# Optimization experiments

Measured on AMD Instinct MI355X. Metric: run time of the kernel, lower is better.

## Reference

```python
import jax, jax.numpy as jnp
import numpy as np

B, F, C, H, W = 4, 16, 768, 16, 16   # video: b f c h w
L, M = 64, 16                        # audio: b c l m
NH = 12                              # num_heads
WS_V = 4                             # local_window (video window size, frames)
GROUPS = 32                          # GroupNorm32
EPS = 1e-5


def group_norm(x, scale, bias):
    # x: [b, c, t]; normalize over (channels-within-group, t)
    b, c, t = x.shape
    xg = x.reshape(b, GROUPS, c // GROUPS, t)
    mu = xg.mean(axis=(2, 3), keepdims=True)
    var = xg.var(axis=(2, 3), keepdims=True)
    xg = (xg - mu) * jax.lax.rsqrt(var + EPS)
    return xg.reshape(b, c, t) * scale[None, :, None] + bias[None, :, None]


def setup_inputs() -> dict:
    key = jax.random.key(0)
    ks = jax.random.split(key, 8)
    s = 0.02
    return {
        "video": jax.random.normal(ks[0], (B, F, C, H, W), jnp.float32),
        "audio": jax.random.normal(ks[1], (B, C, L, M), jnp.float32),
        "vn_scale": jnp.ones((C,), jnp.float32),
        "vn_bias": jnp.zeros((C,), jnp.float32),
        "an_scale": jnp.ones((C,), jnp.float32),
        "an_bias": jnp.zeros((C,), jnp.float32),
        "vqkv_w": jax.random.normal(ks[2], (3 * C, C), jnp.float32) * s,
        "vqkv_b": jnp.zeros((3 * C,), jnp.float32),
        "aqkv_w": jax.random.normal(ks[3], (3 * C, C), jnp.float32) * s,
        "aqkv_b": jnp.zeros((3 * C,), jnp.float32),
        "vproj_w": jax.random.normal(ks[4], (C, C), jnp.float32) * s,  # zero_module in orig; random for nontrivial baseline
        "vproj_b": jnp.zeros((C,), jnp.float32),
        "aproj_w": jax.random.normal(ks[5], (C, C), jnp.float32) * s,
        "aproj_b": jnp.zeros((C,), jnp.float32),
    }


def reference(video, audio, vn_scale, vn_bias, an_scale, an_bias,
              vqkv_w, vqkv_b, aqkv_w, aqkv_b,
              vproj_w, vproj_b, aproj_w, aproj_b):
    b, f, c, h, w = video.shape
    _, _, l, m = audio.shape
    ch = c // NH
    scale = ch ** -0.25
    ws_audio = WS_V * l // f
    nwin = f // WS_V
    wsv_tok = WS_V * h * w      # video tokens per window
    wsa_tok = ws_audio * m      # audio tokens per window

    vt = jnp.transpose(video, (0, 2, 1, 3, 4)).reshape(b, c, f * h * w)  # b c (f h w)
    at = audio.reshape(b, c, l * m)                                       # b c (l m)

    # 1x1 conv qkv after GroupNorm
    vqkv = jnp.einsum('oc,bct->bot', vqkv_w, group_norm(vt, vn_scale, vn_bias)) + vqkv_b[None, :, None]
    aqkv = jnp.einsum('oc,bct->bot', aqkv_w, group_norm(at, an_scale, an_bias)) + aqkv_b[None, :, None]
    q_v, k_v, v_v = jnp.split(vqkv, 3, axis=1)
    q_a, k_a, v_a = jnp.split(aqkv, 3, axis=1)

    # attention_index with window_shift = 0
    va_index = (jnp.arange(wsa_tok)[None, :] + (jnp.arange(nwin) * wsa_tok)[:, None]) % (l * m)
    av_index = (jnp.arange(wsv_tok)[None, :] + (jnp.arange(nwin) * wsv_tok)[:, None]) % (f * h * w)

    def heads(x):
        return x.reshape(b, NH, ch, -1)

    # video queries attend gathered audio windows
    qv = heads(q_v).reshape(b, NH, ch, nwin, wsv_tok)
    ka = jnp.take(heads(k_a), va_index, axis=-1)   # [b,NH,ch,nwin,wsa_tok]
    vav = jnp.take(heads(v_a), va_index, axis=-1)
    wts = jax.nn.softmax(jnp.einsum('bhcnt,bhcns->bhnts', qv * scale, ka * scale), axis=-1)
    v_out = jnp.einsum('bhnts,bhcns->bhcnt', wts, vav).reshape(b, c, f * h * w)

    # audio queries attend gathered video windows
    qa = heads(q_a).reshape(b, NH, ch, nwin, wsa_tok)
    kv = jnp.take(heads(k_v), av_index, axis=-1)   # [b,NH,ch,nwin,wsv_tok]
    vvv = jnp.take(heads(v_v), av_index, axis=-1)
    wts = jax.nn.softmax(jnp.einsum('bhcnt,bhcns->bhnts', qa * scale, kv * scale), axis=-1)
    a_out = jnp.einsum('bhnts,bhcns->bhcnt', wts, vvv).reshape(b, c, l * m)

    # zero-init 1x1x1 / 1x1 proj_out convs + residual
    vh = jnp.transpose(v_out.reshape(b, c, f, h, w), (0, 2, 1, 3, 4))  # b f c h w
    vh = jnp.einsum('oc,bfchw->bfohw', vproj_w, vh) + vproj_b[None, None, :, None, None]
    ah = jnp.einsum('oc,bclm->bolm', aproj_w, a_out.reshape(b, c, l, m)) + aproj_b[None, :, None, None]
    return video + vh, audio + ah
```

## Files before the change

### kernel.cpp

```cpp
#include <hip/hip_runtime.h>
#include <hip/hip_bf16.h>

typedef unsigned short ushort_t;
typedef __attribute__((ext_vector_type(8))) short short8;
typedef __attribute__((ext_vector_type(4))) float f32x4;
struct __align__(8) us4 { ushort_t x, y, z, w; };

#define DI __device__ __forceinline__

DI float b2f(unsigned int u16) {
  union { unsigned int i; float f; } v;
  v.i = u16 << 16;
  return v.f;
}
DI ushort_t f2b(float f) {
  union { float f; unsigned int u; } v; v.f = f;
  unsigned int r = v.u + 0x7FFFu + ((v.u >> 16) & 1u);
  return (ushort_t)(r >> 16);
}

DI void gl_lds16(const ushort_t* g, ushort_t* l) {
  __builtin_amdgcn_global_load_lds(
      (const __attribute__((address_space(1))) unsigned int*)g,
      (__attribute__((address_space(3))) unsigned int*)l, 16, 0, 0);
}

__global__ __launch_bounds__(256) void fused_pre_kernel(
    const float* __restrict__ video, const float* __restrict__ audio,
    float* __restrict__ part,
    const float* __restrict__ w0, const float* __restrict__ w1,
    const float* __restrict__ w2, const float* __restrict__ w3,
    ushort_t* __restrict__ o0, ushort_t* __restrict__ o1,
    ushort_t* __restrict__ o2, ushort_t* __restrict__ o3) {
  const int bid = blockIdx.x;
  const int tid = threadIdx.x;
  __shared__ float red[8];
  if (bid < 2560) {
    float s = 0.f, ss = 0.f;
    if (bid < 2048) {
      int bg = bid >> 4, f = bid & 15;
      int b = bg >> 5, g = bg & 31;
      const float4* base = reinterpret_cast<const float4*>(
          video + ((size_t)((b * 16 + f) * 768 + g * 24)) * 256);
#pragma unroll
      for (int i = 0; i < 6; ++i) {
        float4 v = base[i * 256 + tid];
        s += v.x + v.y + v.z + v.w;
        ss += v.x * v.x + v.y * v.y + v.z * v.z + v.w * v.w;
      }
    } else {
      int a = bid - 2048;
      int bg = a >> 2, p = a & 3;
      int b = bg >> 5, g = bg & 31;
      const float* ab = audio + ((size_t)(b * 768 + g * 24)) * 1024 + p * 256;
#pragma unroll
      for (int i = 0; i < 6; ++i) {
        int row = i * 4 + (tid >> 6);
        float4 v = *reinterpret_cast<const float4*>(ab + (size_t)row * 1024 + (tid & 63) * 4);
        s += v.x + v.y + v.z + v.w;
        ss += v.x * v.x + v.y * v.y + v.z * v.z + v.w * v.w;
      }
    }
    for (int off = 32; off > 0; off >>= 1) { s += __shfl_down(s, off, 64); ss += __shfl_down(ss, off, 64); }
    int wv = tid >> 6, ln = tid & 63;
    if (ln == 0) { red[wv * 2] = s; red[wv * 2 + 1] = ss; }
    __syncthreads();
    if (tid == 0) {
      part[bid * 2] = red[0] + red[2] + red[4] + red[6];
      part[bid * 2 + 1] = red[1] + red[3] + red[5] + red[7];
    }
  } else {
    const int n1 = (2304 * 768) / 4, n3 = (768 * 768) / 4;
    const int total = 2 * n1 + 2 * n3;
    int wb = bid - 2560;
    for (int i = wb * 256 + tid; i < total; i += 1024 * 256) {
      const float4* src;
      ushort_t* dst;
      int j;
      if (i < n1) { src = (const float4*)w0; dst = o0; j = i; }
      else if (i < 2 * n1) { src = (const float4*)w1; dst = o1; j = i - n1; }
      else if (i < 2 * n1 + n3) { src = (const float4*)w2; dst = o2; j = i - 2 * n1; }
      else { src = (const float4*)w3; dst = o3; j = i - 2 * n1 - n3; }
      float4 v = src[j];
      us4 o = {f2b(v.x), f2b(v.y), f2b(v.z), f2b(v.w)};
      *reinterpret_cast<us4*>(dst + (size_t)j * 4) = o;
    }
  }
}

__global__ __launch_bounds__(256) void norm_fused_kernel(
    const float* __restrict__ video, const float* __restrict__ audio,
    const float* __restrict__ part,
    const float* __restrict__ vsc, const float* __restrict__ vbi,
    const float* __restrict__ asc, const float* __restrict__ abi,
    ushort_t* __restrict__ Xv, ushort_t* __restrict__ Xa) {
  __shared__ float T[32][257];
  __shared__ float shA[32], shB[32];
  const int bx = blockIdx.x;
  const int tid = threadIdx.x;
  if (bx < 1536) {
    const int bf = bx / 24, ct = bx % 24;
    const int b = bf >> 4, f = bf & 15;
    const int c0 = ct * 32;
    if (tid < 32) {
      int c = c0 + tid, g = c / 24;
      float s = 0.f, ss = 0.f;
#pragma unroll
      for (int i = 0; i < 16; ++i) {
        s += part[((b * 32 + g) * 16 + i) * 2];
        ss += part[((b * 32 + g) * 16 + i) * 2 + 1];
      }
      const float N = 24.f * 4096.f;
      float m = s / N;
      float r = rsqrtf(ss / N - m * m + 1e-5f);
      float A = r * vsc[c];
      shA[tid] = A;
      shB[tid] = vbi[c] - m * A;
    }
    __syncthreads();
#pragma unroll
    for (int i = 0; i < 8; ++i) {
      int idx = i * 256 + tid;
      int c = idx >> 6, q4 = idx & 63;
      float4 v = *reinterpret_cast<const float4*>(
          video + ((size_t)((b * 16 + f) * 768 + c0 + c)) * 256 + q4 * 4);
      float A = shA[c], B = shB[c];
      float4 o = {A * v.x + B, A * v.y + B, A * v.z + B, A * v.w + B};
      *reinterpret_cast<float4*>(&T[c][q4 * 4]) = o;
    }
    __syncthreads();
#pragma unroll
    for (int i = 0; i < 8; ++i) {
      int idx = i * 256 + tid;
      int c4 = idx & 7, hw = idx >> 3;
      us4 o = {f2b(T[c4 * 4 + 0][hw]), f2b(T[c4 * 4 + 1][hw]),
               f2b(T[c4 * 4 + 2][hw]), f2b(T[c4 * 4 + 3][hw])};
      *reinterpret_cast<us4*>(Xv + ((size_t)(b * 4096 + f * 256 + hw)) * 768 + c0 + c4 * 4) = o;
    }
  } else {
    const int ax = bx - 1536;
    const int bt = ax / 24, ct = ax % 24;
    const int b = bt >> 2, t0 = (bt & 3) * 256;
    const int c0 = ct * 32;
    if (tid < 32) {
      int c = c0 + tid, g = c / 24;
      float s = 0.f, ss = 0.f;
#pragma unroll
      for (int i = 0; i < 4; ++i) {
        s += part[(2048 + (b * 32 + g) * 4 + i) * 2];
        ss += part[(2048 + (b * 32 + g) * 4 + i) * 2 + 1];
      }
      const float N = 24.f * 1024.f;
      float m = s / N;
      float r = rsqrtf(ss / N - m * m + 1e-5f);
      float A = r * asc[c];
      shA[tid] = A;
      shB[tid] = abi[c] - m * A;
    }
    __syncthreads();
#pragma unroll
    for (int i = 0; i < 8; ++i) {
      int idx = i * 256 + tid;
      int c = idx >> 6, q4 = idx & 63;
      float4 v = *reinterpret_cast<const float4*>(
          audio + ((size_t)(b * 768 + c0 + c)) * 1024 + t0 + q4 * 4);
      float A = shA[c], B = shB[c];
      float4 o = {A * v.x + B, A * v.y + B, A * v.z + B, A * v.w + B};
      *reinterpret_cast<float4*>(&T[c][q4 * 4]) = o;
    }
    __syncthreads();
#pragma unroll
    for (int i = 0; i < 8; ++i) {
      int idx = i * 256 + tid;
      int c4 = idx & 7, tt = idx >> 3;
      us4 o = {f2b(T[c4 * 4 + 0][tt]), f2b(T[c4 * 4 + 1][tt]),
               f2b(T[c4 * 4 + 2][tt]), f2b(T[c4 * 4 + 3][tt])};
      *reinterpret_cast<us4*>(Xa + ((size_t)(b * 1024 + t0 + tt)) * 768 + c0 + c4 * 4) = o;
    }
  }
}

__global__ __launch_bounds__(256) void qkv_fused_kernel(
    const ushort_t* __restrict__ Xv, const ushort_t* __restrict__ Xa,
    const ushort_t* __restrict__ Wqv, const ushort_t* __restrict__ Wqa,
    const float* __restrict__ vqkv_b, const float* __restrict__ aqkv_b,
    ushort_t* __restrict__ Qv, ushort_t* __restrict__ Kv, ushort_t* __restrict__ Vv,
    ushort_t* __restrict__ Qa, ushort_t* __restrict__ Ka, ushort_t* __restrict__ Va) {
  __shared__ ushort_t sm[32768];
  const int bid = blockIdx.x;
  const int tid = threadIdx.x;
  const int lane = tid & 63, wave = tid >> 6;
  const int quad = lane >> 4, l16 = lane & 15;

  const bool isv = bid < 2304;
  const int lb = isv ? bid : bid - 2304;
  const int nwg = isv ? 2304 : 576;
  const ushort_t* A = isv ? Xv : Xa;
  const ushort_t* W = isv ? Wqv : Wqa;
  const float* bias = isv ? vqkv_b : aqkv_b;
  ushort_t* pQ = isv ? Qv : Qa;
  ushort_t* pK = isv ? Kv : Ka;
  ushort_t* pV = isv ? Vv : Va;
  const int M = isv ? 16384 : 4096;

  const int lid = (lb & 7) * (nwg >> 3) + (lb >> 3);
  const int n0 = (lid % 18) * 128, m0 = (lid / 18) * 128;
  const int wm = (wave & 1) * 64, wn = (wave >> 1) * 64;

  const int srow = wave * 32 + (lane >> 3);
  const int sq = ((lane & 7) ^ (lane >> 3)) * 8;
  const ushort_t* gA = A + (size_t)(m0 + srow) * 768 + sq;
  const ushort_t* gB = W + (size_t)(n0 + srow) * 768 + sq;

  f32x4 acc[4][4];
#pragma unroll
  for (int i = 0; i < 4; ++i)
#pragma unroll
    for (int j = 0; j < 4; ++j) acc[i][j] = (f32x4){0.f, 0.f, 0.f, 0.f};

  auto stage = [&](int kc, int cur) {
    ushort_t* lA = sm + cur * 8192 + wave * 2048;
    ushort_t* lB = sm + 16384 + cur * 8192 + wave * 2048;
#pragma unroll
    for (int i = 0; i < 4; ++i) {
      gl_lds16(gA + (size_t)i * 8 * 768 + kc, lA + i * 512);
      gl_lds16(gB + (size_t)i * 8 * 768 + kc, lB + i * 512);
    }
  };

  stage(0, 0);
  __syncthreads();
  int cur = 0;
  for (int t = 0; t < 12; ++t) {
    if (t < 11) stage((t + 1) * 64, cur ^ 1);
    const ushort_t* cA = sm + cur * 8192;
    const ushort_t* cB = sm + 16384 + cur * 8192;
#pragma unroll
    for (int ks = 0; ks < 2; ++ks) {
      short8 av[4], bv[4];
#pragma unroll
      for (int im = 0; im < 4; ++im) {
        int rr = wm + im * 16 + l16;
        av[im] = *reinterpret_cast<const short8*>(
            cA + rr * 64 + (((ks * 4 + quad) ^ (rr & 7)) * 8));
      }
#pragma unroll
      for (int in = 0; in < 4; ++in) {
        int rr = wn + in * 16 + l16;
        bv[in] = *reinterpret_cast<const short8*>(
            cB + rr * 64 + (((ks * 4 + quad) ^ (rr & 7)) * 8));
      }
#pragma unroll
      for (int im = 0; im < 4; ++im)
#pragma unroll
        for (int in = 0; in < 4; ++in)
          acc[im][in] = __builtin_amdgcn_mfma_f32_16x16x32_bf16(av[im], bv[in], acc[im][in], 0, 0, 0);
    }
    __syncthreads();
    cur ^= 1;
  }

  ushort_t* sC = sm;
  const int section = n0 / 768;
  const int obase = n0 - section * 768;
  if (section < 2) {
    const float qs = (section == 0) ? 0.125f * 1.44269504088896340736f : 1.0f;
#pragma unroll
    for (int in = 0; in < 4; ++in) {
      int ol = wn + in * 16 + l16;
      float bv_ = bias[n0 + ol];
#pragma unroll
      for (int im = 0; im < 4; ++im)
#pragma unroll
        for (int r = 0; r < 4; ++r) {
          int row = wm + im * 16 + quad * 4 + r;
          sC[row * 136 + ol] = f2b((acc[im][in][r] + bv_) * qs);
        }
    }
    __syncthreads();
    ushort_t* dst = (section == 0) ? pQ : pK;
#pragma unroll
    for (int i = 0; i < 8; ++i) {
      int cid = i * 256 + tid;
      int row = cid >> 4, ch = cid & 15;
      *reinterpret_cast<uint4*>(dst + (size_t)(m0 + row) * 768 + obase + ch * 8) =
          *reinterpret_cast<const uint4*>(sC + row * 136 + ch * 8);
    }
  } else {
#pragma unroll
    for (int in = 0; in < 4; ++in) {
      int ol = wn + in * 16 + l16;
      float bv_ = bias[n0 + ol];
#pragma unroll
      for (int im = 0; im < 4; ++im)
#pragma unroll
        for (int r = 0; r < 4; ++r) {
          int mr = wm + im * 16 + quad * 4 + r;
          sC[ol * 136 + mr] = f2b(acc[im][in][r] + bv_);
        }
    }
    __syncthreads();
#pragma unroll
    for (int i = 0; i < 8; ++i) {
      int cid = i * 256 + tid;
      int o = cid >> 4, ch = cid & 15;
      *reinterpret_cast<uint4*>(pV + (size_t)(obase + o) * M + m0 + ch * 8) =
          *reinterpret_cast<const uint4*>(sC + o * 136 + ch * 8);
    }
  }
}

__global__ __launch_bounds__(256) void proj_fused_kernel(
    const ushort_t* __restrict__ Ov, const ushort_t* __restrict__ Oa,
    const ushort_t* __restrict__ Wpv, const ushort_t* __restrict__ Wpa,
    const float* __restrict__ vproj_b, const float* __restrict__ aproj_b,
    float* __restrict__ out_v, const float* __restrict__ video,
    float* __restrict__ out_a, const float* __restrict__ audio) {
  __shared__ ushort_t sm[32768];
  const int bid = blockIdx.x;
  const int tid = threadIdx.x;
  const int lane = tid & 63, wave = tid >> 6;
  const int quad = lane >> 4, l16 = lane & 15;

  const bool isv = bid < 768;
  const int lb = isv ? bid : bid - 768;
  const int nwg = isv ? 768 : 192;
  const ushort_t* A = isv ? Ov : Oa;
  const ushort_t* W = isv ? Wpv : Wpa;
  const float* bias = isv ? vproj_b : aproj_b;
  float* outp = isv ? out_v : out_a;
  const float* resp = isv ? video : audio;

  const int lid = (lb & 7) * (nwg >> 3) + (lb >> 3);
  const int n0 = (lid % 6) * 128, m0 = (lid / 6) * 128;
  const int wm = (wave & 1) * 64, wn = (wave >> 1) * 64;

  const int srow = wave * 32 + (lane >> 3);
  const int sq = ((lane & 7) ^ (lane >> 3)) * 8;
  const ushort_t* gA = A + (size_t)(m0 + srow) * 768 + sq;
  const ushort_t* gB = W + (size_t)(n0 + srow) * 768 + sq;

  f32x4 acc[4][4];
#pragma unroll
  for (int i = 0; i < 4; ++i)
#pragma unroll
    for (int j = 0; j < 4; ++j) acc[i][j] = (f32x4){0.f, 0.f, 0.f, 0.f};

  auto stage = [&](int kc, int cur) {
    ushort_t* lA = sm + cur * 8192 + wave * 2048;
    ushort_t* lB = sm + 16384 + cur * 8192 + wave * 2048;
#pragma unroll
    for (int i = 0; i < 4; ++i) {
      gl_lds16(gA + (size_t)i * 8 * 768 + kc, lA + i * 512);
      gl_lds16(gB + (size_t)i * 8 * 768 + kc, lB + i * 512);
    }
  };

  stage(0, 0);
  __syncthreads();
  int cur = 0;
  for (int t = 0; t < 12; ++t) {
    if (t < 11) stage((t + 1) * 64, cur ^ 1);
    const ushort_t* cA = sm + cur * 8192;
    const ushort_t* cB = sm + 16384 + cur * 8192;
#pragma unroll
    for (int ks = 0; ks < 2; ++ks) {
      short8 av[4], bv[4];
#pragma unroll
      for (int im = 0; im < 4; ++im) {
        int rr = wm + im * 16 + l16;
        av[im] = *reinterpret_cast<const short8*>(
            cA + rr * 64 + (((ks * 4 + quad) ^ (rr & 7)) * 8));
      }
#pragma unroll
      for (int in = 0; in < 4; ++in) {
        int rr = wn + in * 16 + l16;
        bv[in] = *reinterpret_cast<const short8*>(
            cB + rr * 64 + (((ks * 4 + quad) ^ (rr & 7)) * 8));
      }
#pragma unroll
      for (int im = 0; im < 4; ++im)
#pragma unroll
        for (int in = 0; in < 4; ++in)
          acc[im][in] = __builtin_amdgcn_mfma_f32_16x16x32_bf16(av[im], bv[in], acc[im][in], 0, 0, 0);
    }
    __syncthreads();
    cur ^= 1;
  }

  ushort_t* sC = sm;
#pragma unroll
  for (int in = 0; in < 4; ++in) {
    int ol = wn + in * 16 + l16;
    float bv_ = bias[n0 + ol];
#pragma unroll
    for (int im = 0; im < 4; ++im)
#pragma unroll
      for (int r = 0; r < 4; ++r) {
        int mr = wm + im * 16 + quad * 4 + r;
        sC[ol * 136 + mr] = f2b(acc[im][in][r] + bv_);
      }
  }
  __syncthreads();
#pragma unroll
  for (int i = 0; i < 16; ++i) {
    int cid = i * 256 + tid;
    int o = cid >> 5, ch = cid & 31;
    uint2 pk = *reinterpret_cast<const uint2*>(sC + o * 136 + ch * 4);
    size_t gidx;
    if (isv) {
      int b = m0 >> 12, f = (m0 >> 8) & 15, hw0 = m0 & 255;
      gidx = ((size_t)((b * 16 + f) * 768 + n0 + o)) * 256 + hw0 + ch * 4;
    } else {
      int b = m0 >> 10, t0 = m0 & 1023;
      gidx = ((size_t)(b * 768 + n0 + o)) * 1024 + t0 + ch * 4;
    }
    float4 rv = *reinterpret_cast<const float4*>(resp + gidx);
    float4 ov;
    ov.x = rv.x + b2f(pk.x & 0xffff);
    ov.y = rv.y + b2f(pk.x >> 16);
    ov.z = rv.z + b2f(pk.y & 0xffff);
    ov.w = rv.w + b2f(pk.y >> 16);
    *reinterpret_cast<float4*>(outp + gidx) = ov;
  }
}

__global__ __launch_bounds__(512) void attn_fused_kernel(
    const ushort_t* __restrict__ Qv, const ushort_t* __restrict__ Ka,
    const ushort_t* __restrict__ Va, ushort_t* __restrict__ Ov,
    const ushort_t* __restrict__ Qa, const ushort_t* __restrict__ Kv,
    const ushort_t* __restrict__ Vv, ushort_t* __restrict__ Oa) {
  __shared__ ushort_t sm[33792];
  ushort_t* sK = sm;
  ushort_t* sV = sm + 8192;
  ushort_t* sP = sm + 16384;
  const int tid = threadIdx.x;
  const int lane = tid & 63, wave = tid >> 6;
  const int quad = lane >> 4, l16 = lane & 15;
  const int half = wave >> 2, w4 = wave & 3;
  ushort_t* sPh = sP + half * 8704;
  ushort_t* sQh = sPh;

  const int bx0 = blockIdx.x;
  const bool isv = bx0 >= 384;
  int lb;
  if (isv) {
    int local = bx0 - 384;
    lb = (local & 7) * 192 + (local >> 3);
  } else {
    int local = bx0;
    lb = (local & 7) * 48 + (local >> 3);
  }

  const ushort_t* Qt = isv ? Qv : Qa;
  const ushort_t* Kt = isv ? Ka : Kv;
  const ushort_t* Vc = isv ? Va : Vv;
  ushort_t* Ot = isv ? Ov : Oa;
  const int qlog = isv ? 3 : 1;
  const int NT = isv ? 2 : 8;
  const int QW = isv ? 1024 : 256;
  const int SW = isv ? 256 : 1024;
  const int TQb = isv ? 4096 : 1024;
  const int TSb = isv ? 1024 : 4096;
  const int Ms = isv ? 4096 : 16384;

  const int qt = lb & ((1 << qlog) - 1);
  const int win = (lb >> qlog) & 3;
  const int whb = lb >> (qlog + 2);
  const int h = whb % 12;
  const int batch = whb / 12;
  const int hc = h * 64;
  const int nq0 = batch * TQb + win * QW + qt * 128;
  const int ns_base = batch * TSb + win * SW;

  const int r8 = lane >> 3, c8 = lane & 7;
  const int s8 = (c8 ^ r8) * 8;
  const int r16 = lane >> 4, c16 = lane & 15;

  auto stage_k = [&](int ns0) {
#pragma unroll
    for (int i = 0; i < 2; ++i) {
      int rbase = wave * 16 + i * 8;
      gl_lds16(Kt + (size_t)(ns0 + rbase + r8) * 768 + hc + s8, sK + rbase * 64);
    }
  };
  auto stage_v = [&](int ns0) {
#pragma unroll
    for (int i = 0; i < 2; ++i) {
      int cbase = wave * 8 + i * 4;
      int ch = cbase + r16;
      int slot = c16 ^ (ch & 15);
      gl_lds16(Vc + (size_t)(hc + ch) * Ms + ns0 + slot * 8, sV + cbase * 128);
    }
  };

#pragma unroll
  for (int i = 0; i < 2; ++i) {
    int rbase = wave * 16 + i * 8;
    gl_lds16(Qt + (size_t)(nq0 + rbase + r8) * 768 + hc + s8,
             sP + (rbase >> 6) * 8704 + (rbase & 63) * 64);
  }
  stage_k(ns_base);
  stage_v(ns_base);
  __syncthreads();

  short8 qf[2];
#pragma unroll
  for (int ks = 0; ks < 2; ++ks)
    qf[ks] = *reinterpret_cast<const short8*>(
        sQh + (w4 * 16 + l16) * 64 + (((ks * 4 + quad) ^ (l16 & 7)) * 8));

  const short8 vones = {0x3F80, 0x3F80, 0x3F80, 0x3F80, 0x3F80, 0x3F80, 0x3F80, 0x3F80};

  float mr[4];
  f32x4 on[4], onl;
#pragma unroll
  for (int r = 0; r < 4; ++r) mr[r] = -1e30f;
#pragma unroll
  for (int nc = 0; nc < 4; ++nc) on[nc] = (f32x4){0.f, 0.f, 0.f, 0.f};
  onl = (f32x4){0.f, 0.f, 0.f, 0.f};
  const int prow0 = (w4 * 16 + quad * 4) * 136;

  for (int t = 0; t < NT; ++t) {
    f32x4 sf[8];
#pragma unroll
    for (int nt = 0; nt < 8; ++nt) sf[nt] = (f32x4){0.f, 0.f, 0.f, 0.f};
    __builtin_amdgcn_s_setprio(1);
#pragma unroll
    for (int ks = 0; ks < 2; ++ks) {
#pragma unroll
      for (int nt = 0; nt < 8; ++nt) {
        short8 kf = *reinterpret_cast<const short8*>(
            sK + (nt * 16 + l16) * 64 + (((ks * 4 + quad) ^ (l16 & 7)) * 8));
        sf[nt] = __builtin_amdgcn_mfma_f32_16x16x32_bf16(qf[ks], kf, sf[nt], 0, 0, 0);
      }
    }
    __builtin_amdgcn_s_setprio(0);
    __syncthreads();
    if (t + 1 < NT) stage_k(ns_base + (t + 1) * 128);
#pragma unroll
    for (int r = 0; r < 4; ++r) {
      float m_ = fmaxf(fmaxf(sf[0][r], sf[1][r]), sf[2][r]);
      m_ = fmaxf(fmaxf(m_, sf[3][r]), sf[4][r]);
      m_ = fmaxf(fmaxf(m_, sf[5][r]), sf[6][r]);
      m_ = fmaxf(m_, sf[7][r]);
#pragma unroll
      for (int off = 1; off < 16; off <<= 1) m_ = fmaxf(m_, __shfl_xor(m_, off));
      float mnew = fmaxf(mr[r], m_);
      float al = __builtin_amdgcn_exp2f(mr[r] - mnew);
      mr[r] = mnew;
      int prow = prow0 + r * 136;
#pragma unroll
      for (int nt = 0; nt < 8; ++nt) {
        float p = __builtin_amdgcn_exp2f(sf[nt][r] - mnew);
        sPh[prow + nt * 16 + l16] = (ushort_t)((__float_as_uint(p) + 0x8000u) >> 16);
      }
#pragma unroll
      for (int nc = 0; nc < 4; ++nc) on[nc][r] *= al;
      onl[r] *= al;
    }
    __builtin_amdgcn_s_setprio(1);
#pragma unroll
    for (int ks = 0; ks < 4; ++ks) {
      short8 pf = *reinterpret_cast<const short8*>(sPh + (w4 * 16 + l16) * 136 + ks * 32 + quad * 8);
#pragma unroll
      for (int nc = 0; nc < 4; ++nc) {
        short8 vf = *reinterpret_cast<const short8*>(
            sV + (nc * 16 + l16) * 128 + (((ks * 4 + quad) ^ l16) * 8));
        on[nc] = __builtin_amdgcn_mfma_f32_16x16x32_bf16(pf, vf, on[nc], 0, 0, 0);
      }
      onl = __builtin_amdgcn_mfma_f32_16x16x32_bf16(pf, vones, onl, 0, 0, 0);
    }
    __builtin_amdgcn_s_setprio(0);
    if (t + 1 < NT) {
      __syncthreads();
      stage_v(ns_base + (t + 1) * 128);
    }
  }
#pragma unroll
  for (int r = 0; r < 4; ++r) {
    float inv = 1.f / onl[r];
    int prow = prow0 + r * 136;
#pragma unroll
    for (int nc = 0; nc < 4; ++nc)
      sPh[prow + nc * 16 + l16] = f2b(on[nc][r] * inv);
  }
  __syncthreads();
#pragma unroll
  for (int i = 0; i < 2; ++i) {
    int c = i * 512 + tid;
    int row = c >> 3, cc = c & 7;
    *reinterpret_cast<uint4*>(Ot + (size_t)(nq0 + row) * 768 + hc + cc * 8) =
        *reinterpret_cast<const uint4*>(sP + (row >> 6) * 8704 + (row & 63) * 136 + cc * 8);
  }
}

extern "C" void kernel_launch(void* const* d_in, const int* in_sizes, int n_in,
                              void* d_out, int out_size, void* d_ws, size_t ws_size,
                              hipStream_t stream) {
  (void)in_sizes; (void)n_in; (void)out_size; (void)ws_size;
  const float* video = (const float*)d_in[0];
  const float* audio = (const float*)d_in[1];
  const float* vn_s = (const float*)d_in[2];
  const float* vn_b = (const float*)d_in[3];
  const float* an_s = (const float*)d_in[4];
  const float* an_b = (const float*)d_in[5];
  const float* vqkv_w = (const float*)d_in[6];
  const float* vqkv_b = (const float*)d_in[7];
  const float* aqkv_w = (const float*)d_in[8];
  const float* aqkv_b = (const float*)d_in[9];
  const float* vproj_w = (const float*)d_in[10];
  const float* vproj_b = (const float*)d_in[11];
  const float* aproj_w = (const float*)d_in[12];
  const float* aproj_b = (const float*)d_in[13];

  float* out_v = (float*)d_out;
  float* out_a = out_v + (size_t)4 * 16 * 768 * 16 * 16;

  char* ws = (char*)d_ws;
  size_t off = 0;
  auto carve = [&](size_t bytes) {
    char* p = ws + off;
    off += (bytes + 255) & ~(size_t)255;
    return p;
  };
  float* part = (float*)carve(2560 * 2 * 4);
  ushort_t* Xv = (ushort_t*)carve((size_t)16384 * 768 * 2);
  ushort_t* Xa = (ushort_t*)carve((size_t)4096 * 768 * 2);
  ushort_t* Wqv = (ushort_t*)carve((size_t)2304 * 768 * 2);
  ushort_t* Wqa = (ushort_t*)carve((size_t)2304 * 768 * 2);
  ushort_t* Wpv = (ushort_t*)carve((size_t)768 * 768 * 2);
  ushort_t* Wpa = (ushort_t*)carve((size_t)768 * 768 * 2);
  ushort_t* Qv = (ushort_t*)carve((size_t)16384 * 768 * 2);
  ushort_t* Kv = (ushort_t*)carve((size_t)16384 * 768 * 2);
  ushort_t* Vv = (ushort_t*)carve((size_t)16384 * 768 * 2);
  ushort_t* Qa = (ushort_t*)carve((size_t)4096 * 768 * 2);
  ushort_t* Ka = (ushort_t*)carve((size_t)4096 * 768 * 2);
  ushort_t* Va = (ushort_t*)carve((size_t)4096 * 768 * 2);
  ushort_t* Ov = Xv;
  ushort_t* Oa = Xa;

  fused_pre_kernel<<<3584, 256, 0, stream>>>(video, audio, part,
                                             vqkv_w, aqkv_w, vproj_w, aproj_w,
                                             Wqv, Wqa, Wpv, Wpa);
  norm_fused_kernel<<<1920, 256, 0, stream>>>(video, audio, part,
                                              vn_s, vn_b, an_s, an_b, Xv, Xa);
  qkv_fused_kernel<<<2880, 256, 0, stream>>>(Xv, Xa, Wqv, Wqa, vqkv_b, aqkv_b,
                                             Qv, Kv, Vv, Qa, Ka, Va);
  attn_fused_kernel<<<1920, 512, 0, stream>>>(Qv, Ka, Va, Ov, Qa, Kv, Vv, Oa);
  proj_fused_kernel<<<960, 256, 0, stream>>>(Ov, Oa, Wpv, Wpa, vproj_b, aproj_b,
                                             out_v, video, out_a, audio);
}
```

Baseline: 321.9 us.

## Enlarge QKV GEMM tiles to 256x256 with 512-thread workgroups

The QKV projection GEMM moves from 128x128 tiles with 4 waves to 256x256 tiles with 8 waves. Each wave now computes 128x64, and LDS grows to 128KB for double-buffered A/B. The larger tile raises arithmetic intensity and cuts redundant global loads of X and W. In exchange there are fewer workgroups (720 vs 256 CUs, about 2.8 waves per CU), higher register pressure from the 8x4 accumulators, lower occupancy, and an epilogue split into two halves with extra barriers.

```diff
diff --git a/kernel.cpp b/kernel.cpp
--- a/kernel.cpp
+++ b/kernel.cpp
@@ -180,21 +180,21 @@
   }
 }
 
-__global__ __launch_bounds__(256) void qkv_fused_kernel(
+__global__ __launch_bounds__(512) void qkv_fused_kernel(
     const ushort_t* __restrict__ Xv, const ushort_t* __restrict__ Xa,
     const ushort_t* __restrict__ Wqv, const ushort_t* __restrict__ Wqa,
     const float* __restrict__ vqkv_b, const float* __restrict__ aqkv_b,
     ushort_t* __restrict__ Qv, ushort_t* __restrict__ Kv, ushort_t* __restrict__ Vv,
     ushort_t* __restrict__ Qa, ushort_t* __restrict__ Ka, ushort_t* __restrict__ Va) {
-  __shared__ ushort_t sm[32768];
+  __shared__ ushort_t sm[65536];
   const int bid = blockIdx.x;
   const int tid = threadIdx.x;
   const int lane = tid & 63, wave = tid >> 6;
   const int quad = lane >> 4, l16 = lane & 15;
 
-  const bool isv = bid < 2304;
-  const int lb = isv ? bid : bid - 2304;
-  const int nwg = isv ? 2304 : 576;
+  const bool isv = bid < 576;
+  const int lb = isv ? bid : bid - 576;
+  const int seg8 = isv ? 72 : 18;
   const ushort_t* A = isv ? Xv : Xa;
   const ushort_t* W = isv ? Wqv : Wqa;
   const float* bias = isv ? vqkv_b : aqkv_b;
@@ -203,28 +203,28 @@
   ushort_t* pV = isv ? Vv : Va;
   const int M = isv ? 16384 : 4096;
 
-  const int lid = (lb & 7) * (nwg >> 3) + (lb >> 3);
-  const int n0 = (lid % 18) * 128, m0 = (lid / 18) * 128;
-  const int wm = (wave & 1) * 64, wn = (wave >> 1) * 64;
-
-  const int srow = wave * 32 + (lane >> 3);
-  const int sq = ((lane & 7) ^ (lane >> 3)) * 8;
-  const ushort_t* gA = A + (size_t)(m0 + srow) * 768 + sq;
-  const ushort_t* gB = W + (size_t)(n0 + srow) * 768 + sq;
-
-  f32x4 acc[4][4];
-#pragma unroll
-  for (int i = 0; i < 4; ++i)
+  const int lid = (lb & 7) * seg8 + (lb >> 3);
+  const int n0 = (lid % 9) * 256, m0 = (lid / 9) * 256;
+  const int wm = (wave & 1) * 128, wn = (wave >> 1) * 64;
+
+  const int r8 = lane >> 3;
+  const int sq = ((lane & 7) ^ r8) * 8;
+  const ushort_t* gA = A + (size_t)(m0 + wave * 8 + r8) * 768 + sq;
+  const ushort_t* gB = W + (size_t)(n0 + wave * 8 + r8) * 768 + sq;
+
+  f32x4 acc[8][4];
+#pragma unroll
+  for (int i = 0; i < 8; ++i)
 #pragma unroll
     for (int j = 0; j < 4; ++j) acc[i][j] = (f32x4){0.f, 0.f, 0.f, 0.f};
 
   auto stage = [&](int kc, int cur) {
-    ushort_t* lA = sm + cur * 8192 + wave * 2048;
-    ushort_t* lB = sm + 16384 + cur * 8192 + wave * 2048;
+    ushort_t* lA = sm + cur * 16384 + wave * 512;
+    ushort_t* lB = sm + 32768 + cur * 16384 + wave * 512;
 #pragma unroll
     for (int i = 0; i < 4; ++i) {
-      gl_lds16(gA + (size_t)i * 8 * 768 + kc, lA + i * 512);
-      gl_lds16(gB + (size_t)i * 8 * 768 + kc, lB + i * 512);
+      gl_lds16(gA + (size_t)i * 64 * 768 + kc, lA + i * 4096);
+      gl_lds16(gB + (size_t)i * 64 * 768 + kc, lB + i * 4096);
     }
   };
 
@@ -233,17 +233,11 @@
   int cur = 0;
   for (int t = 0; t < 12; ++t) {
     if (t < 11) stage((t + 1) * 64, cur ^ 1);
-    const ushort_t* cA = sm + cur * 8192;
-    const ushort_t* cB = sm + 16384 + cur * 8192;
+    const ushort_t* cA = sm + cur * 16384;
+    const ushort_t* cB = sm + 32768 + cur * 16384;
 #pragma unroll
     for (int ks = 0; ks < 2; ++ks) {
-      short8 av[4], bv[4];
-#pragma unroll
-      for (int im = 0; im < 4; ++im) {
-        int rr = wm + im * 16 + l16;
-        av[im] = *reinterpret_cast<const short8*>(
-            cA + rr * 64 + (((ks * 4 + quad) ^ (rr & 7)) * 8));
-      }
+      short8 bv[4];
 #pragma unroll
       for (int in = 0; in < 4; ++in) {
         int rr = wn + in * 16 + l16;
@@ -251,10 +245,14 @@
             cB + rr * 64 + (((ks * 4 + quad) ^ (rr & 7)) * 8));
       }
 #pragma unroll
-      for (int im = 0; im < 4; ++im)
+      for (int im = 0; im < 8; ++im) {
+        int rr = wm + im * 16 + l16;
+        short8 av = *reinterpret_cast<const short8*>(
+            cA + rr * 64 + (((ks * 4 + quad) ^ (rr & 7)) * 8));
 #pragma unroll
         for (int in = 0; in < 4; ++in)
-          acc[im][in] = __builtin_amdgcn_mfma_f32_16x16x32_bf16(av[im], bv[in], acc[im][in], 0, 0, 0);
+          acc[im][in] = __builtin_amdgcn_mfma_f32_16x16x32_bf16(av, bv[in], acc[im][in], 0, 0, 0);
+      }
     }
     __syncthreads();
     cur ^= 1;
@@ -265,47 +263,60 @@
   const int obase = n0 - section * 768;
   if (section < 2) {
     const float qs = (section == 0) ? 0.125f * 1.44269504088896340736f : 1.0f;
-#pragma unroll
-    for (int in = 0; in < 4; ++in) {
-      int ol = wn + in * 16 + l16;
-      float bv_ = bias[n0 + ol];
-#pragma unroll
-      for (int im = 0; im < 4; ++im)
-#pragma unroll
-        for (int r = 0; r < 4; ++r) {
-          int row = wm + im * 16 + quad * 4 + r;
-          sC[row * 136 + ol] = f2b((acc[im][in][r] + bv_) * qs);
+    ushort_t* dst = (section == 0) ? pQ : pK;
+#pragma unroll
+    for (int chh = 0; chh < 2; ++chh) {
+      if ((wn >> 7) == chh) {
+#pragma unroll
+        for (int in = 0; in < 4; ++in) {
+          int ol = wn + in * 16 + l16;
+          float bv_ = bias[n0 + ol];
+          int olh = ol & 127;
+#pragma unroll
+          for (int im = 0; im < 8; ++im)
+#pragma unroll
+            for (int r = 0; r < 4; ++r) {
+              int row = wm + im * 16 + quad * 4 + r;
+              sC[row * 136 + olh] = f2b((acc[im][in][r] + bv_) * qs);
+            }
         }
-    }
-    __syncthreads();
-    ushort_t* dst = (section == 0) ? pQ : pK;
-#pragma unroll
-    for (int i = 0; i < 8; ++i) {
-      int cid = i * 256 + tid;
-      int row = cid >> 4, ch = cid & 15;
-      *reinterpret_cast<uint4*>(dst + (size_t)(m0 + row) * 768 + obase + ch * 8) =
-          *reinterpret_cast<const uint4*>(sC + row * 136 + ch * 8);
+      }
+      __syncthreads();
+#pragma unroll
+      for (int i = 0; i < 8; ++i) {
+        int cid = i * 512 + tid;
+        int row = cid >> 4, ck = cid & 15;
+        *reinterpret_cast<uint4*>(dst + (size_t)(m0 + row) * 768 + obase + chh * 128 + ck * 8) =
+            *reinterpret_cast<const uint4*>(sC + row * 136 + ck * 8);
+      }
+      __syncthreads();
     }
   } else {
 #pragma unroll
-    for (int in = 0; in < 4; ++in) {
-      int ol = wn + in * 16 + l16;
-      float bv_ = bias[n0 + ol];
-#pragma unroll
-      for (int im = 0; im < 4; ++im)
-#pragma unroll
-        for (int r = 0; r < 4; ++r) {
-          int mr = wm + im * 16 + quad * 4 + r;
-          sC[ol * 136 + mr] = f2b(acc[im][in][r] + bv_);
+    for (int mh = 0; mh < 2; ++mh) {
+      if ((wm >> 7) == mh) {
+#pragma unroll
+        for (int in = 0; in < 4; ++in) {
+          int ol = wn + in * 16 + l16;
+          float bv_ = bias[n0 + ol];
+#pragma unroll
+          for (int im = 0; im < 8; ++im)
+#pragma unroll
+            for (int r = 0; r < 4; ++r) {
+              int row = im * 16 + quad * 4 + r;
+              sC[ol * 136 + row] = f2b(acc[im][in][r] + bv_);
+            }
         }
-    }
-    __syncthreads();
-#pragma unroll
-    for (int i = 0; i < 8; ++i) {
-      int cid = i * 256 + tid;
-      int o = cid >> 4, ch = cid & 15;
-      *reinterpret_cast<uint4*>(pV + (size_t)(obase + o) * M + m0 + ch * 8) =
-          *reinterpret_cast<const uint4*>(sC + o * 136 + ch * 8);
+      }
+      __syncthreads();
+#pragma unroll
+      for (int i = 0; i < 8; ++i) {
+        int cid = i * 512 + tid;
+        int o = cid >> 4, ck = cid & 15;
+        *reinterpret_cast<uint4*>(pV + (size_t)(obase + o) * M + m0 + mh * 128 + ck * 8) =
+            *reinterpret_cast<const uint4*>(sC + o * 136 + ck * 8);
+      }
+      __syncthreads();
     }
   }
 }
@@ -645,8 +656,8 @@
                                              Wqv, Wqa, Wpv, Wpa);
   norm_fused_kernel<<<1920, 256, 0, stream>>>(video, audio, part,
                                               vn_s, vn_b, an_s, an_b, Xv, Xa);
-  qkv_fused_kernel<<<2880, 256, 0, stream>>>(Xv, Xa, Wqv, Wqa, vqkv_b, aqkv_b,
-                                             Qv, Kv, Vv, Qa, Ka, Va);
+  qkv_fused_kernel<<<720, 512, 0, stream>>>(Xv, Xa, Wqv, Wqa, vqkv_b, aqkv_b,
+                                            Qv, Kv, Vv, Qa, Ka, Va);
   attn_fused_kernel<<<1920, 512, 0, stream>>>(Qv, Ka, Va, Ov, Qa, Kv, Vv, Oa);
   proj_fused_kernel<<<960, 256, 0, stream>>>(Ov, Oa, Wpv, Wpa, vproj_b, aproj_b,
                                              out_v, video, out_a, audio);
```

New measurement: 333.5 us. 1.04x slower.
